# Kernel optimization log

Measured on AMD Instinct MI355X. Metric: run time of the kernel, lower is better.

Reference implementation:

```python
import jax, jax.numpy as jnp
import numpy as np

FP8_MAX = 448.0   # E4M3 max finite value
AMAX_EPS = 1e-8
MOMENTUM = 0.95


def _compute_scale(amax):
    return FP8_MAX / jnp.clip(amax, AMAX_EPS)


def _fp8_cast_ste(t, scale):
    """clamp(t*scale, +-448) -> fp8_e4m3 -> back to t.dtype, /scale. STE grad."""
    s = scale.astype(jnp.float32)
    t_scaled = jnp.clip(t.astype(jnp.float32) * s, -FP8_MAX, FP8_MAX)
    t_deq = t_scaled.astype(jnp.float8_e4m3fn).astype(t.dtype) / s.astype(t.dtype)
    # straight-through: forward value = t_deq, gradient = identity wrt t
    return t + jax.lax.stop_gradient(t_deq - t)


def _update_amax(buf, new_amax):
    new_amax = jnp.nan_to_num(new_amax, nan=AMAX_EPS, posinf=FP8_MAX, neginf=AMAX_EPS)
    return jnp.clip(jnp.maximum(buf * MOMENTUM, new_amax), AMAX_EPS)


def setup_inputs() -> dict:
    key = jax.random.key(0)
    k1, k2, k3 = jax.random.split(key, 3)
    x = jax.random.normal(k1, (8192, 4096), dtype=jnp.float32)
    weight = jax.random.normal(k2, (4096, 4096), dtype=jnp.float32) * 0.02
    bias = jax.random.normal(k3, (4096,), dtype=jnp.float32) * 0.01
    input_amax = jnp.ones((), dtype=jnp.float32)
    weight_amax = jnp.ones((), dtype=jnp.float32)
    return {"x": x, "weight": weight, "bias": bias,
            "input_amax": input_amax, "weight_amax": weight_amax}


def reference(x, weight, bias, input_amax, weight_amax):
    # delayed scaling: scales from previous-step amax buffers
    x_scale = _compute_scale(input_amax).astype(jnp.float32)
    w_scale = _compute_scale(weight_amax).astype(jnp.float32)
    x2 = x.reshape(-1, weight.shape[1])  # [T, in]
    x_q = _fp8_cast_ste(x2, x_scale)
    w_q = _fp8_cast_ste(weight, w_scale)
    out = jnp.einsum('ti,oi->to', x_q, w_q) + bias  # [T, out]
    # amax EMA updates (buffers)
    new_input_amax = _update_amax(input_amax, jnp.max(jnp.abs(x2)))
    new_weight_amax = _update_amax(weight_amax, jnp.max(jnp.abs(weight)))
    return out, new_input_amax, new_weight_amax
```

## Files before the change

### kernel.cpp

```cpp
#include <hip/hip_runtime.h>
#include <cstdint>
#include <cstddef>

#define FP8_MAXV 448.0f
#define AMAX_EPS 1e-8f
#define MOMENTUM 0.95f

#define M_DIM 8192
#define N_DIM 4096
#define K_DIM 4096

#define XBLOCKS 2048
#define WBLOCKS 1024

typedef float f32x4 __attribute__((ext_vector_type(4)));

__device__ __forceinline__ void gload_lds16(const void* g, void* l) {
  __builtin_amdgcn_global_load_lds(
      (const __attribute__((address_space(1))) void*)g,
      (__attribute__((address_space(3))) void*)l, 16, 0, 0);
}

__global__ __launch_bounds__(256) void k_quant(
    const float* __restrict__ x, const float* __restrict__ w,
    unsigned int* __restrict__ xq, unsigned int* __restrict__ wq,
    const float* __restrict__ ax_buf, const float* __restrict__ aw_buf,
    float* __restrict__ xpart, float* __restrict__ wpart) {
  const float* in;
  unsigned int* outq;
  float* part;
  int bid, nblocks, n4;
  float sc;
  if (blockIdx.x < XBLOCKS) {
    in = x; outq = xq; part = xpart;
    bid = blockIdx.x; nblocks = XBLOCKS; n4 = (M_DIM * K_DIM) / 4;
    sc = FP8_MAXV / fmaxf(ax_buf[0], AMAX_EPS);
  } else {
    in = w; outq = wq; part = wpart;
    bid = blockIdx.x - XBLOCKS; nblocks = WBLOCKS; n4 = (N_DIM * K_DIM) / 4;
    sc = FP8_MAXV / fmaxf(aw_buf[0], AMAX_EPS);
  }
  float lm = 0.0f;
  const int stride = nblocks * 256;
  for (int i = bid * 256 + threadIdx.x; i < n4; i += stride) {
    float4 v = ((const float4*)in)[i];
    lm = fmaxf(lm, fmaxf(fmaxf(fabsf(v.x), fabsf(v.y)),
                         fmaxf(fabsf(v.z), fabsf(v.w))));
    float a0 = fminf(fmaxf(v.x * sc, -FP8_MAXV), FP8_MAXV);
    float a1 = fminf(fmaxf(v.y * sc, -FP8_MAXV), FP8_MAXV);
    float a2 = fminf(fmaxf(v.z * sc, -FP8_MAXV), FP8_MAXV);
    float a3 = fminf(fmaxf(v.w * sc, -FP8_MAXV), FP8_MAXV);
    int p = 0;
    p = __builtin_amdgcn_cvt_pk_fp8_f32(a0, a1, p, false);
    p = __builtin_amdgcn_cvt_pk_fp8_f32(a2, a3, p, true);
    outq[i] = (unsigned int)p;
  }
  #pragma unroll
  for (int off = 32; off > 0; off >>= 1)
    lm = fmaxf(lm, __shfl_down(lm, off));
  __shared__ float smax[4];
  if ((threadIdx.x & 63) == 0) smax[threadIdx.x >> 6] = lm;
  __syncthreads();
  if (threadIdx.x == 0)
    part[bid] = fmaxf(fmaxf(smax[0], smax[1]), fmaxf(smax[2], smax[3]));
}

__global__ __launch_bounds__(256, 2) void k_gemm(
    const unsigned char* __restrict__ Aq, const unsigned char* __restrict__ Bq,
    const float* __restrict__ bias,
    const float* __restrict__ ax_buf, const float* __restrict__ aw_buf,
    const float* __restrict__ xpart, const float* __restrict__ wpart,
    float* __restrict__ out) {
  __shared__ __align__(16) unsigned char ldsA[128 * 64];
  __shared__ __align__(16) unsigned char ldsB[128 * 64];

  const int tid = threadIdx.x;
  const int w = tid >> 6;
  const int l = tid & 63;
  const int m = l & 15;
  const int q = l >> 4;
  const int qh = q >> 1;
  const int ql = q & 1;
  const int wr = (w >> 1) * 64;
  const int wc = (w & 1) * 64;
  const int blockRow = blockIdx.y * 128;
  const int blockCol = blockIdx.x * 128;

  const int c0 = w * 2;
  const int srow = c0 * 16 + (l >> 2);
  const int sgrp = (l & 3) ^ ((l >> 2) & 3) ^ ((l >> 4) & 3);
  const int scol = sgrp * 16;
  const unsigned char* gA = Aq + (size_t)(blockRow + srow) * K_DIM + scol;
  const unsigned char* gB = Bq + (size_t)(blockCol + srow) * K_DIM + scol;
  unsigned char* lA = &ldsA[c0 * 1024];
  unsigned char* lB = &ldsB[c0 * 1024];

  const int f = (m & 3) ^ ((m >> 2) & 3);

  f32x4 acc[4][4] = {};

  for (int k0 = 0; k0 < K_DIM; k0 += 64) {
    gload_lds16(gA + k0, lA);
    gload_lds16(gA + k0 + (size_t)16 * K_DIM, lA + 1024);
    gload_lds16(gB + k0, lB);
    gload_lds16(gB + k0 + (size_t)16 * K_DIM, lB + 1024);
    __syncthreads();
    #pragma unroll
    for (int s = 0; s < 2; ++s) {
      const int off = (((2 * s + qh) ^ f) * 16) + ql * 8;
      long a[4], b[4];
      #pragma unroll
      for (int i = 0; i < 4; ++i)
        a[i] = *(const long*)(ldsA + (wr + i * 16 + m) * 64 + off);
      #pragma unroll
      for (int j = 0; j < 4; ++j)
        b[j] = *(const long*)(ldsB + (wc + j * 16 + m) * 64 + off);
      #pragma unroll
      for (int i = 0; i < 4; ++i)
        #pragma unroll
        for (int j = 0; j < 4; ++j)
          acc[i][j] = __builtin_amdgcn_mfma_f32_16x16x32_fp8_fp8(
              a[i], b[j], acc[i][j], 0, 0, 0);
    }
    __syncthreads();
  }

  const float inv = fmaxf(ax_buf[0], AMAX_EPS) * fmaxf(aw_buf[0], AMAX_EPS) *
                    (1.0f / (FP8_MAXV * FP8_MAXV));

  #pragma unroll
  for (int j = 0; j < 4; ++j) {
    const int colg = blockCol + wc + j * 16 + m;
    const float bv = bias[colg];
    #pragma unroll
    for (int i = 0; i < 4; ++i) {
      const int rowg = blockRow + wr + i * 16 + q * 4;
      #pragma unroll
      for (int r = 0; r < 4; ++r)
        out[(size_t)(rowg + r) * N_DIM + colg] = acc[i][j][r] * inv + bv;
    }
  }

  if (blockIdx.x == 0 && blockIdx.y == 0) {
    float mx = 0.0f, mw = 0.0f;
    for (int i = tid; i < XBLOCKS; i += 256) mx = fmaxf(mx, xpart[i]);
    for (int i = tid; i < WBLOCKS; i += 256) mw = fmaxf(mw, wpart[i]);
    #pragma unroll
    for (int off = 32; off > 0; off >>= 1) {
      mx = fmaxf(mx, __shfl_down(mx, off));
      mw = fmaxf(mw, __shfl_down(mw, off));
    }
    __syncthreads();
    float* red = (float*)ldsA;
    if (l == 0) { red[w] = mx; red[4 + w] = mw; }
    __syncthreads();
    if (tid == 0) {
      mx = fmaxf(fmaxf(red[0], red[1]), fmaxf(red[2], red[3]));
      mw = fmaxf(fmaxf(red[4], red[5]), fmaxf(red[6], red[7]));
      float* tail = out + (size_t)M_DIM * N_DIM;
      tail[0] = fmaxf(fmaxf(ax_buf[0] * MOMENTUM, mx), AMAX_EPS);
      tail[1] = fmaxf(fmaxf(aw_buf[0] * MOMENTUM, mw), AMAX_EPS);
    }
  }
}

extern "C" void kernel_launch(void* const* d_in, const int* in_sizes, int n_in,
                              void* d_out, int out_size, void* d_ws, size_t ws_size,
                              hipStream_t stream) {
  const float* x      = (const float*)d_in[0];
  const float* weight = (const float*)d_in[1];
  const float* bias   = (const float*)d_in[2];
  const float* in_ax  = (const float*)d_in[3];
  const float* in_aw  = (const float*)d_in[4];
  float* out = (float*)d_out;

  float* xpart = (float*)d_ws;
  float* wpart = xpart + XBLOCKS;
  unsigned char* xq = (unsigned char*)d_ws + 16384;
  unsigned char* wq = xq + (size_t)M_DIM * K_DIM;

  k_quant<<<XBLOCKS + WBLOCKS, 256, 0, stream>>>(
      x, weight, (unsigned int*)xq, (unsigned int*)wq, in_ax, in_aw,
      xpart, wpart);

  dim3 grid(N_DIM / 128, M_DIM / 128);
  k_gemm<<<grid, 256, 0, stream>>>(xq, wq, bias, in_ax, in_aw,
                                   xpart, wpart, out);
}
```

Baseline: 446.2 us.

## Switch GEMM to scaled 16x16x128 FP8 MFMA with 128-wide K tiles

Replaces the 16x16x32 FP8 MFMA with the gfx950 scaled 16x16x128 f8f6f4 MFMA using unit scales, and doubles the K tile to 128 bytes per row with a new 8-way XOR swizzle and 128-bit LDS reads. This gives fewer MFMA instructions, fewer K-loop iterations and fewer barriers per output tile. LDS use doubles to 32KB per block, which may limit occupancy. The operand layout has to match the instruction's expected lane mapping for results to stay correct.

After: 407.9 us. 8.6% less time.

```diff
diff --git a/kernel.cpp b/kernel.cpp
--- a/kernel.cpp
+++ b/kernel.cpp
@@ -13,7 +13,11 @@
 #define XBLOCKS 2048
 #define WBLOCKS 1024
 
+#define SCALE_ONE 0x7F7F7F7F
+
 typedef float f32x4 __attribute__((ext_vector_type(4)));
+typedef int   i32x4 __attribute__((ext_vector_type(4)));
+typedef int   i32x8 __attribute__((ext_vector_type(8)));
 
 __device__ __forceinline__ void gload_lds16(const void* g, void* l) {
   __builtin_amdgcn_global_load_lds(
@@ -71,57 +75,61 @@
     const float* __restrict__ ax_buf, const float* __restrict__ aw_buf,
     const float* __restrict__ xpart, const float* __restrict__ wpart,
     float* __restrict__ out) {
-  __shared__ __align__(16) unsigned char ldsA[128 * 64];
-  __shared__ __align__(16) unsigned char ldsB[128 * 64];
+  __shared__ __align__(16) unsigned char ldsA[128 * 128];
+  __shared__ __align__(16) unsigned char ldsB[128 * 128];
 
   const int tid = threadIdx.x;
   const int w = tid >> 6;
   const int l = tid & 63;
   const int m = l & 15;
   const int q = l >> 4;
-  const int qh = q >> 1;
-  const int ql = q & 1;
   const int wr = (w >> 1) * 64;
   const int wc = (w & 1) * 64;
   const int blockRow = blockIdx.y * 128;
   const int blockCol = blockIdx.x * 128;
 
-  const int c0 = w * 2;
-  const int srow = c0 * 16 + (l >> 2);
-  const int sgrp = (l & 3) ^ ((l >> 2) & 3) ^ ((l >> 4) & 3);
-  const int scol = sgrp * 16;
-  const unsigned char* gA = Aq + (size_t)(blockRow + srow) * K_DIM + scol;
-  const unsigned char* gB = Bq + (size_t)(blockCol + srow) * K_DIM + scol;
-  unsigned char* lA = &ldsA[c0 * 1024];
-  unsigned char* lB = &ldsB[c0 * 1024];
+  const int srow = l >> 3;
+  const int sgrp = (l & 7) ^ srow;
+  const unsigned char* gA =
+      Aq + (size_t)(blockRow + w * 32 + srow) * K_DIM + sgrp * 16;
+  const unsigned char* gB =
+      Bq + (size_t)(blockCol + w * 32 + srow) * K_DIM + sgrp * 16;
+  unsigned char* lA = &ldsA[w * 4096];
+  unsigned char* lB = &ldsB[w * 4096];
 
-  const int f = (m & 3) ^ ((m >> 2) & 3);
-
+  const int mk = m & 7;
   f32x4 acc[4][4] = {};
 
-  for (int k0 = 0; k0 < K_DIM; k0 += 64) {
-    gload_lds16(gA + k0, lA);
-    gload_lds16(gA + k0 + (size_t)16 * K_DIM, lA + 1024);
-    gload_lds16(gB + k0, lB);
-    gload_lds16(gB + k0 + (size_t)16 * K_DIM, lB + 1024);
+  for (int k0 = 0; k0 < K_DIM; k0 += 128) {
+    #pragma unroll
+    for (int cc = 0; cc < 4; ++cc) {
+      gload_lds16(gA + k0 + (size_t)(cc * 8) * K_DIM, lA + cc * 1024);
+      gload_lds16(gB + k0 + (size_t)(cc * 8) * K_DIM, lB + cc * 1024);
+    }
     __syncthreads();
+
+    i32x8 a[4], b[4];
     #pragma unroll
-    for (int s = 0; s < 2; ++s) {
-      const int off = (((2 * s + qh) ^ f) * 16) + ql * 8;
-      long a[4], b[4];
-      #pragma unroll
-      for (int i = 0; i < 4; ++i)
-        a[i] = *(const long*)(ldsA + (wr + i * 16 + m) * 64 + off);
+    for (int i = 0; i < 4; ++i) {
+      const unsigned char* p = ldsA + (wr + i * 16 + m) * 128;
+      i32x4 lo = *(const i32x4*)(p + (((2 * q) ^ mk) * 16));
+      i32x4 hi = *(const i32x4*)(p + (((2 * q + 1) ^ mk) * 16));
+      a[i] = __builtin_shufflevector(lo, hi, 0, 1, 2, 3, 4, 5, 6, 7);
+    }
+    #pragma unroll
+    for (int j = 0; j < 4; ++j) {
+      const unsigned char* p = ldsB + (wc + j * 16 + m) * 128;
+      i32x4 lo = *(const i32x4*)(p + (((2 * q) ^ mk) * 16));
+      i32x4 hi = *(const i32x4*)(p + (((2 * q + 1) ^ mk) * 16));
+      b[j] = __builtin_shufflevector(lo, hi, 0, 1, 2, 3, 4, 5, 6, 7);
+    }
+    #pragma unroll
+    for (int i = 0; i < 4; ++i)
       #pragma unroll
       for (int j = 0; j < 4; ++j)
-        b[j] = *(const long*)(ldsB + (wc + j * 16 + m) * 64 + off);
-      #pragma unroll
-      for (int i = 0; i < 4; ++i)
-        #pragma unroll
-        for (int j = 0; j < 4; ++j)
-          acc[i][j] = __builtin_amdgcn_mfma_f32_16x16x32_fp8_fp8(
-              a[i], b[j], acc[i][j], 0, 0, 0);
-    }
+        acc[i][j] = __builtin_amdgcn_mfma_scale_f32_16x16x128_f8f6f4(
+            a[i], b[j], acc[i][j],  0,  0,
+             0, SCALE_ONE,  0, SCALE_ONE);
     __syncthreads();
   }
 
```
